# Kernel optimization log

Measured on AMD Instinct MI355X. Metric: run time of the kernel, lower is better.

The kernel has to match this reference:

```python
import jax, jax.numpy as jnp
import numpy as np

N_NODES = 50000
N_EDGES = 800000
IN_CH, HID, OUT_CH = 128, 256, 40


def setup_inputs() -> dict:
    key = jax.random.key(0)
    ks = jax.random.split(key, 10)
    x = jax.random.normal(ks[0], (N_NODES, IN_CH), dtype=jnp.float32)
    edge_index = jax.random.randint(ks[1], (2, N_EDGES), 0, N_NODES, dtype=jnp.int64)
    s = 0.05  # weight init scale
    return {
        "x": x,
        "edge_index": edge_index,
        "W1a": jax.random.normal(ks[2], (IN_CH, HID), dtype=jnp.float32) * s,
        "b1a": jnp.zeros((HID,), jnp.float32),
        "W2a": jax.random.normal(ks[3], (HID, HID), dtype=jnp.float32) * s,
        "b2a": jnp.zeros((HID,), jnp.float32),
        "W1b": jax.random.normal(ks[4], (HID, HID), dtype=jnp.float32) * s,
        "b1b": jnp.zeros((HID,), jnp.float32),
        "W2b": jax.random.normal(ks[5], (HID, HID), dtype=jnp.float32) * s,
        "b2b": jnp.zeros((HID,), jnp.float32),
        "Wlin": jax.random.normal(ks[6], (HID * 2, OUT_CH), dtype=jnp.float32) * s,
        "blin": jnp.zeros((OUT_CH,), jnp.float32),
    }


def _gin_conv(h, src, dst, W1, b1, W2, b2):
    # sum-aggregate messages h[src] into destination nodes, eps = 0
    agg = jax.ops.segment_sum(h[src], dst, num_segments=N_NODES)
    z = h + agg
    z = jnp.maximum(z @ W1 + b1, 0.0) @ W2 + b2  # 2-layer MLP
    return z


def reference(x, edge_index, W1a, b1a, W2a, b2a, W1b, b1b, W2b, b2b, Wlin, blin):
    src, dst = edge_index[0], edge_index[1]
    h1 = jnp.maximum(_gin_conv(x, src, dst, W1a, b1a, W2a, b2a), 0.0)
    h2 = jnp.maximum(_gin_conv(h1, src, dst, W1b, b1b, W2b, b2b), 0.0)
    h_cat = jnp.concatenate([h1, h2], axis=1)  # [N, 2*HID]
    logits = h_cat @ Wlin + blin
    return jax.nn.log_softmax(logits, axis=1)
```

## Files before the change

kernel.cpp:

```cpp
#include <hip/hip_runtime.h>
#include <math.h>

#define N_NODES 50000
#define N_EDGES 800000
#define IN_CH 128
#define HID 256
#define OUT_CH 40
#define GRP 6250
#define NCHUNK 64
#define TS 264

typedef unsigned short u16;
typedef unsigned char u8;
typedef __attribute__((ext_vector_type(8))) short bf16x8;
typedef __attribute__((ext_vector_type(8))) unsigned short u16x8;
typedef __attribute__((ext_vector_type(4))) float f32x4;
typedef __attribute__((ext_vector_type(2))) float f32x2;

__device__ __forceinline__ float bf2f(u16 u) {
    union { unsigned int i; float f; } v; v.i = ((unsigned int)u) << 16; return v.f;
}
__device__ __forceinline__ u16 f2bf(float f) {
    union { float f; unsigned int i; } v; v.f = f;
    unsigned int x = v.i;
    x += 0x7fffu + ((x >> 16) & 1u);
    return (u16)(x >> 16);
}

#define GLOBAL_AS __attribute__((address_space(1)))
#define LDS_AS __attribute__((address_space(3)))
__device__ __forceinline__ void async_cp16(const void* g, void* l) {
    __builtin_amdgcn_global_load_lds((const GLOBAL_AS unsigned int*)g,
                                     (LDS_AS unsigned int*)l, 16, 0, 0);
}

__device__ __forceinline__ void pack_w(
    const float* __restrict__ in, u16* __restrict__ out, int K, int N, int c)
{
    for (int k = threadIdx.x; k < K; k += 256) {
        int kk32 = k >> 5, quad = (k >> 3) & 3, e = k & 7;
        size_t base = (((size_t)c * (K >> 5) + kk32) * 64 + quad * 16) * 8 + e;
#pragma unroll
        for (int li = 0; li < 16; li++) {
            int n = c * 16 + li;
            float v = (n < N) ? in[(size_t)k * N + n] : 0.f;
            out[base + (size_t)li * 8] = f2bf(v);
        }
    }
}

__global__ __launch_bounds__(256) void prep_fused(
    const float* __restrict__ x, u16* __restrict__ xb, u8* __restrict__ xf8,
    const int* __restrict__ ei, u16* __restrict__ e16,
    const float* __restrict__ W1a, const float* __restrict__ W2a,
    const float* __restrict__ W1b, const float* __restrict__ W2b,
    const float* __restrict__ Wlin,
    u16* __restrict__ W1aPk, u16* __restrict__ W2aPk,
    u16* __restrict__ W1bPk, u16* __restrict__ W2bPk, u16* __restrict__ WlinPk)
{
    int b = blockIdx.x;
    if (b < 6250) {
        int i = b * 256 + threadIdx.x;
        float4 v = ((const float4*)x)[i];
        ushort4 o;
        o.x = f2bf(v.x); o.y = f2bf(v.y); o.z = f2bf(v.z); o.w = f2bf(v.w);
        ((ushort4*)xb)[i] = o;
        int p = __builtin_amdgcn_cvt_pk_fp8_f32(v.x, v.y, 0, false);
        p = __builtin_amdgcn_cvt_pk_fp8_f32(v.z, v.w, p, true);
        ((unsigned int*)xf8)[i] = (unsigned int)p;
    } else if (b < 7813) {
        int i = (b - 6250) * 256 + threadIdx.x;
        if (i < (2 * N_EDGES) / 4) {
            int4 v = ((const int4*)ei)[i];
            ushort4 o;
            o.x = (u16)v.x; o.y = (u16)v.y; o.z = (u16)v.z; o.w = (u16)v.w;
            ((ushort4*)e16)[i] = o;
        }
    } else {
        int t = b - 7813;
        if (t < 16)       pack_w(W1a, W1aPk, IN_CH, HID, t);
        else if (t < 32)  pack_w(W2a, W2aPk, HID, HID, t - 16);
        else if (t < 48)  pack_w(W1b, W1bPk, HID, HID, t - 32);
        else if (t < 64)  pack_w(W2b, W2bPk, HID, HID, t - 48);
        else              pack_w(Wlin, WlinPk, 2 * HID, OUT_CH, t - 64);
    }
}

__global__ __launch_bounds__(256) void hist_priv(
    const u16* __restrict__ dst16, u16* __restrict__ partial)
{
    __shared__ int hist[GRP];
    const int b = blockIdx.x;
    const int g = b & 7;
    const int sub = b >> 3;
    const int lo = g * GRP;
    const int CH = N_EDGES / NCHUNK;
    for (int i = threadIdx.x; i < GRP; i += 256) hist[i] = 0;
    __syncthreads();
    const ushort4* dsts = (const ushort4*)(dst16 + sub * CH);
    for (int k = threadIdx.x; k < CH / 4; k += 256) {
        ushort4 d = dsts[k];
        int r0 = (int)d.x - lo, r1 = (int)d.y - lo;
        int r2 = (int)d.z - lo, r3 = (int)d.w - lo;
        if ((unsigned)r0 < (unsigned)GRP) atomicAdd(&hist[r0], 1);
        if ((unsigned)r1 < (unsigned)GRP) atomicAdd(&hist[r1], 1);
        if ((unsigned)r2 < (unsigned)GRP) atomicAdd(&hist[r2], 1);
        if ((unsigned)r3 < (unsigned)GRP) atomicAdd(&hist[r3], 1);
    }
    __syncthreads();
    u16* po = partial + (size_t)b * GRP;
    for (int i = threadIdx.x; i < GRP; i += 256) po[i] = (u16)hist[i];
}

__global__ __launch_bounds__(256) void scan1(
    const u16* __restrict__ partial, int* __restrict__ excl,
    int* __restrict__ partials_out)
{
    __shared__ int lds[256];
    const int tid = threadIdx.x;
    const int base = blockIdx.x * 1024 + tid * 4;
    int v[4]; int s = 0;
#pragma unroll
    for (int i = 0; i < 4; i++) {
        int idx = base + i;
        int d = 0;
        if (idx < N_NODES) {
            int g = idx / GRP;
            int off = idx - g * GRP;
#pragma unroll
            for (int sub = 0; sub < NCHUNK; sub++)
                d += partial[(size_t)(sub * 8 + g) * GRP + off];
        }
        v[i] = d;
        s += d;
    }
    lds[tid] = s;
    __syncthreads();
    for (int off = 1; off < 256; off <<= 1) {
        int t = (tid >= off) ? lds[tid - off] : 0;
        __syncthreads();
        lds[tid] += t;
        __syncthreads();
    }
    int run = lds[tid] - s;
#pragma unroll
    for (int i = 0; i < 4; i++) {
        int idx = base + i;
        if (idx < N_NODES) excl[idx] = run;
        run += v[i];
    }
    if (tid == 255) partials_out[blockIdx.x] = lds[255];
}

__global__ __launch_bounds__(256) void scan3(
    int* __restrict__ excl, const int* __restrict__ partials,
    int* __restrict__ cursor, int nPart)
{
    __shared__ int bp[64];
    const int tid = threadIdx.x;
    if (tid < 64) {
        int orig = (tid < nPart) ? partials[tid] : 0;
        int v = orig;
#pragma unroll
        for (int off = 1; off < 64; off <<= 1) {
            int t = __shfl_up(v, off, 64);
            if (tid >= off) v += t;
        }
        bp[tid] = v - orig;
    }
    __syncthreads();
    int idx = blockIdx.x * 256 + tid;
    if (idx < N_NODES) {
        int r = excl[idx] + bp[idx >> 10];
        excl[idx] = r;
        cursor[idx] = r;
    }
}

__global__ __launch_bounds__(256) void csr_fill(
    const u16* __restrict__ src16, const u16* __restrict__ dst16,
    int* __restrict__ cursor, u16* __restrict__ csr_src)
{
    const int g = blockIdx.x & 7;
    const int c = blockIdx.x >> 3;
    const int lo = g * GRP, hi = lo + GRP;
    const int base = c * 2048;
#pragma unroll
    for (int i = 0; i < 8; i++) {
        int e = base + i * 256 + threadIdx.x;
        if (e < N_EDGES) {
            int d = dst16[e];
            if (d >= lo && d < hi) {
                int pos = atomicAdd(&cursor[d], 1);
                csr_src[pos] = src16[e];
            }
        }
    }
}


__global__ __launch_bounds__(256) void gather_agg_f8_128(
    const u16* __restrict__ feat_bf, const u8* __restrict__ feat_f8,
    const int* __restrict__ row_ptr, const int* __restrict__ row_end,
    const u16* __restrict__ csr_src, u16* __restrict__ out)
{
    const int tid = threadIdx.x;
    const int lane = tid & 63;
    const int wv = tid >> 6;
    const int li = lane & 7;
    int node = blockIdx.x * 32 + wv * 8 + (lane >> 3);
    const bool valid = node < N_NODES;
    if (!valid) node = N_NODES - 1;

    int j = row_ptr[node];
    int deg = valid ? (row_end[node] - j) : 0;

    float acc[16];
    {
        u16x8 s0 = *(const u16x8*)(feat_bf + (size_t)node * IN_CH + li * 16);
        u16x8 s1 = *(const u16x8*)(feat_bf + (size_t)node * IN_CH + li * 16 + 8);
#pragma unroll
        for (int q = 0; q < 8; q++) { acc[q] = bf2f(s0[q]); acc[8 + q] = bf2f(s1[q]); }
    }

    int maxdeg = deg;
#pragma unroll
    for (int off = 8; off < 64; off <<= 1)
        maxdeg = max(maxdeg, __shfl_xor(maxdeg, off, 64));

    for (int it = 0; it < maxdeg; it += 4) {
        int4 g0 = {0,0,0,0}, g1 = {0,0,0,0}, g2 = {0,0,0,0}, g3 = {0,0,0,0};
        if (it < deg)
            g0 = *(const int4*)(feat_f8 + (size_t)csr_src[j + it] * IN_CH + li * 16);
        if (it + 1 < deg)
            g1 = *(const int4*)(feat_f8 + (size_t)csr_src[j + it + 1] * IN_CH + li * 16);
        if (it + 2 < deg)
            g2 = *(const int4*)(feat_f8 + (size_t)csr_src[j + it + 2] * IN_CH + li * 16);
        if (it + 3 < deg)
            g3 = *(const int4*)(feat_f8 + (size_t)csr_src[j + it + 3] * IN_CH + li * 16);
#pragma unroll
        for (int q = 0; q < 4; q++) {
            int w0 = (&g0.x)[q], w1 = (&g1.x)[q], w2 = (&g2.x)[q], w3 = (&g3.x)[q];
            f32x2 l0 = __builtin_amdgcn_cvt_pk_f32_fp8(w0, false);
            f32x2 h0 = __builtin_amdgcn_cvt_pk_f32_fp8(w0, true);
            f32x2 l1 = __builtin_amdgcn_cvt_pk_f32_fp8(w1, false);
            f32x2 h1 = __builtin_amdgcn_cvt_pk_f32_fp8(w1, true);
            f32x2 l2 = __builtin_amdgcn_cvt_pk_f32_fp8(w2, false);
            f32x2 h2 = __builtin_amdgcn_cvt_pk_f32_fp8(w2, true);
            f32x2 l3 = __builtin_amdgcn_cvt_pk_f32_fp8(w3, false);
            f32x2 h3 = __builtin_amdgcn_cvt_pk_f32_fp8(w3, true);
            acc[q * 4 + 0] += (l0.x + l1.x) + (l2.x + l3.x);
            acc[q * 4 + 1] += (l0.y + l1.y) + (l2.y + l3.y);
            acc[q * 4 + 2] += (h0.x + h1.x) + (h2.x + h3.x);
            acc[q * 4 + 3] += (h0.y + h1.y) + (h2.y + h3.y);
        }
    }

    if (valid) {
        u16x8 o0, o1;
#pragma unroll
        for (int q = 0; q < 8; q++) { o0[q] = f2bf(acc[q]); o1[q] = f2bf(acc[8 + q]); }
        *(u16x8*)(out + (size_t)node * IN_CH + li * 16) = o0;
        *(u16x8*)(out + (size_t)node * IN_CH + li * 16 + 8) = o1;
    }
}

__global__ __launch_bounds__(256) void gather_agg_f8_256(
    const u16* __restrict__ feat_bf, const u8* __restrict__ feat_f8,
    const int* __restrict__ row_ptr, const int* __restrict__ row_end,
    const u16* __restrict__ csr_src, u16* __restrict__ out)
{
    const int tid = threadIdx.x;
    const int lane = tid & 63;
    const int wv = tid >> 6;
    const int li = lane & 15;
    const int node = blockIdx.x * 16 + wv * 4 + (lane >> 4);

    int j = row_ptr[node];
    int deg = row_end[node] - j;

    float acc[16];
    {
        u16x8 s0 = *(const u16x8*)(feat_bf + (size_t)node * HID + li * 16);
        u16x8 s1 = *(const u16x8*)(feat_bf + (size_t)node * HID + li * 16 + 8);
#pragma unroll
        for (int q = 0; q < 8; q++) { acc[q] = bf2f(s0[q]); acc[8 + q] = bf2f(s1[q]); }
    }

    int maxdeg = deg;
#pragma unroll
    for (int off = 16; off < 64; off <<= 1)
        maxdeg = max(maxdeg, __shfl_xor(maxdeg, off, 64));

    for (int it = 0; it < maxdeg; it += 4) {
        int4 g0 = {0,0,0,0}, g1 = {0,0,0,0}, g2 = {0,0,0,0}, g3 = {0,0,0,0};
        if (it < deg)
            g0 = *(const int4*)(feat_f8 + (size_t)csr_src[j + it] * HID + li * 16);
        if (it + 1 < deg)
            g1 = *(const int4*)(feat_f8 + (size_t)csr_src[j + it + 1] * HID + li * 16);
        if (it + 2 < deg)
            g2 = *(const int4*)(feat_f8 + (size_t)csr_src[j + it + 2] * HID + li * 16);
        if (it + 3 < deg)
            g3 = *(const int4*)(feat_f8 + (size_t)csr_src[j + it + 3] * HID + li * 16);
#pragma unroll
        for (int q = 0; q < 4; q++) {
            int w0 = (&g0.x)[q], w1 = (&g1.x)[q], w2 = (&g2.x)[q], w3 = (&g3.x)[q];
            f32x2 l0 = __builtin_amdgcn_cvt_pk_f32_fp8(w0, false);
            f32x2 h0 = __builtin_amdgcn_cvt_pk_f32_fp8(w0, true);
            f32x2 l1 = __builtin_amdgcn_cvt_pk_f32_fp8(w1, false);
            f32x2 h1 = __builtin_amdgcn_cvt_pk_f32_fp8(w1, true);
            f32x2 l2 = __builtin_amdgcn_cvt_pk_f32_fp8(w2, false);
            f32x2 h2 = __builtin_amdgcn_cvt_pk_f32_fp8(w2, true);
            f32x2 l3 = __builtin_amdgcn_cvt_pk_f32_fp8(w3, false);
            f32x2 h3 = __builtin_amdgcn_cvt_pk_f32_fp8(w3, true);
            acc[q * 4 + 0] += (l0.x + l1.x) + (l2.x + l3.x);
            acc[q * 4 + 1] += (l0.y + l1.y) + (l2.y + l3.y);
            acc[q * 4 + 2] += (h0.x + h1.x) + (h2.x + h3.x);
            acc[q * 4 + 3] += (h0.y + h1.y) + (h2.y + h3.y);
        }
    }

    u16x8 o0, o1;
#pragma unroll
    for (int q = 0; q < 8; q++) { o0[q] = f2bf(acc[q]); o1[q] = f2bf(acc[8 + q]); }
    *(u16x8*)(out + (size_t)node * HID + li * 16) = o0;
    *(u16x8*)(out + (size_t)node * HID + li * 16 + 8) = o1;
}

__global__ __launch_bounds__(256, 4) void mlp_fused(
    const u16* __restrict__ A, int K1,
    const u16* __restrict__ W1pk, const float* __restrict__ b1,
    const u16* __restrict__ W2pk, const float* __restrict__ b2,
    u16* __restrict__ out, u8* __restrict__ outF8, int M)
{
    __shared__ u16 SB[64 * TS];

    const int tid = threadIdx.x;
    const int lane = tid & 63;
    const int wid = tid >> 6;
    const int li = lane & 15;
    const int quad = lane >> 4;
    const int koff = quad * 8;
    const int row0 = blockIdx.x * 64;
    const int KB1 = K1 >> 5;
    const int rsh = (K1 == 256) ? 9 : 8;

    {
        const u8* Ag = (const u8*)(A + (size_t)row0 * K1);
        const int rounds = K1 >> 5;
        for (int j = 0; j < rounds; j++) {
            int L = (j * 256 + tid) * 16;
            int G = L ^ (((L >> rsh) & 7) << 4);
            async_cp16(Ag + G, (u8*)SB + L);
        }
    }

    f32x4 acc[4][4];
#pragma unroll
    for (int i = 0; i < 4; i++)
#pragma unroll
        for (int j = 0; j < 4; j++) acc[i][j] = (f32x4){0.f, 0.f, 0.f, 0.f};

#define LDW(WF, WPK, KB, KK32)                                                \
    {   _Pragma("unroll")                                                     \
        for (int t = 0; t < 4; t++)                                           \
            WF[t] = *(const bf16x8*)((WPK) +                                  \
                (((size_t)(wid * 4 + t) * (KB) + (KK32)) * 64 + lane) * 8); }
#define LDA1(AF, KK)                                                          \
    {   _Pragma("unroll")                                                     \
        for (int t = 0; t < 4; t++) {                                         \
            int row = t * 16 + li;                                            \
            int bo = row * (K1 * 2) + ((KK) + koff) * 2;                      \
            bo ^= (row & 7) << 4;                                             \
            AF[t] = *(const bf16x8*)((const u8*)SB + bo); } }
#define LDA2(AF, KK)                                                          \
    {   _Pragma("unroll")                                                     \
        for (int t = 0; t < 4; t++)                                           \
            AF[t] = *(const bf16x8*)(SB + (t * 16 + li) * TS + (KK) + koff); }
#define MFMA16(AF, WF)                                                        \
    {   _Pragma("unroll")                                                     \
        for (int mt = 0; mt < 4; mt++)                                        \
            _Pragma("unroll")                                                 \
            for (int nt = 0; nt < 4; nt++)                                    \
                acc[mt][nt] = __builtin_amdgcn_mfma_f32_16x16x32_bf16(        \
                    AF[mt], WF[nt], acc[mt][nt], 0, 0, 0); }

    bf16x8 wfA[4], wfB[4], af[4];

    LDW(wfA, W1pk, KB1, 0);
    __syncthreads();

    for (int kk32 = 0; kk32 < KB1; kk32 += 2) {
        LDW(wfB, W1pk, KB1, kk32 + 1);
        LDA1(af, kk32 * 32);
        MFMA16(af, wfA);
        if (kk32 + 2 < KB1) LDW(wfA, W1pk, KB1, kk32 + 2);
        LDA1(af, kk32 * 32 + 32);
        MFMA16(af, wfB);
    }
    __syncthreads();

#pragma unroll
    for (int nt = 0; nt < 4; nt++) {
        int col = wid * 64 + nt * 16 + li;
        float bv = b1[col];
#pragma unroll
        for (int mt = 0; mt < 4; mt++) {
#pragma unroll
            for (int reg = 0; reg < 4; reg++) {
                int row = mt * 16 + quad * 4 + reg;
                float v = fmaxf(acc[mt][nt][reg] + bv, 0.f);
                SB[row * TS + col] = f2bf(v);
                acc[mt][nt][reg] = 0.f;
            }
        }
    }
    LDW(wfA, W2pk, 8, 0);
    __syncthreads();

    for (int kk32 = 0; kk32 < 8; kk32 += 2) {
        LDW(wfB, W2pk, 8, kk32 + 1);
        LDA2(af, kk32 * 32);
        MFMA16(af, wfA);
        if (kk32 + 2 < 8) LDW(wfA, W2pk, 8, kk32 + 2);
        LDA2(af, kk32 * 32 + 32);
        MFMA16(af, wfB);
    }
#undef LDW
#undef LDA1
#undef LDA2
#undef MFMA16

    __syncthreads();
#pragma unroll
    for (int nt = 0; nt < 4; nt++) {
        int col = wid * 64 + nt * 16 + li;
        float bv = b2[col];
#pragma unroll
        for (int mt = 0; mt < 4; mt++) {
#pragma unroll
            for (int reg = 0; reg < 4; reg++) {
                int row = mt * 16 + quad * 4 + reg;
                float v = fmaxf(acc[mt][nt][reg] + bv, 0.f);
                SB[row * TS + col] = f2bf(v);
            }
        }
    }
    __syncthreads();
#pragma unroll
    for (int it = 0; it < 8; it++) {
        int flat = it * 4096 + tid * 16;
        int r = flat >> 9;
        int cu = (flat & 511) >> 1;
        int row = row0 + r;
        if (row < M) {
            u16x8 v = *(const u16x8*)(SB + r * TS + cu);
            *(u16x8*)(out + (size_t)row * HID + cu) = v;
            if (outF8 != nullptr) {
                int p0 = __builtin_amdgcn_cvt_pk_fp8_f32(bf2f(v[0]), bf2f(v[1]), 0, false);
                p0 = __builtin_amdgcn_cvt_pk_fp8_f32(bf2f(v[2]), bf2f(v[3]), p0, true);
                int p1 = __builtin_amdgcn_cvt_pk_fp8_f32(bf2f(v[4]), bf2f(v[5]), 0, false);
                p1 = __builtin_amdgcn_cvt_pk_fp8_f32(bf2f(v[6]), bf2f(v[7]), p1, true);
                int2 pv; pv.x = p0; pv.y = p1;
                *(int2*)(outF8 + (size_t)row * HID + cu) = pv;
            }
        }
    }
}

__global__ __launch_bounds__(256, 6) void gemm_mfma(
    const u16* __restrict__ A, const u16* __restrict__ Acat, int Ksplit, int ldA,
    const u16* __restrict__ Bpk, const float* __restrict__ bias,
    float* __restrict__ out, int M, int K)
{
    const int tid = threadIdx.x;
    const int lane = tid & 63;
    const int wid = tid >> 6;
    const int li = lane & 15;
    const int quad = lane >> 4;
    const int koff = quad * 8;
    const int row0 = blockIdx.x * 64 + wid * 16;

    f32x4 acc[3];
#pragma unroll
    for (int i = 0; i < 3; i++) acc[i] = (f32x4){0.f, 0.f, 0.f, 0.f};

    int r = row0 + li;
    const int arow = (r < M) ? r : (M - 1);
    const int KB = K >> 5;

#define LD_G(AF, BF, KK)                                                      \
    {   const u16* Ab = ((KK) >= Ksplit) ? Acat : A;                          \
        const int kb = ((KK) >= Ksplit) ? ((KK) - Ksplit) : (KK);             \
        AF = *(const bf16x8*)(Ab + (size_t)arow * ldA + kb + koff);           \
        _Pragma("unroll")                                                     \
        for (int t = 0; t < 3; t++)                                           \
            BF[t] = *(const bf16x8*)(Bpk +                                    \
                (((size_t)t * KB + ((KK) >> 5)) * 64 + lane) * 8); }
#define MFMA3(AF, BF)                                                         \
    {   _Pragma("unroll")                                                     \
        for (int nt = 0; nt < 3; nt++)                                        \
            acc[nt] = __builtin_amdgcn_mfma_f32_16x16x32_bf16(                \
                AF, BF[nt], acc[nt], 0, 0, 0); }

    {
        bf16x8 a0, b0[3], a1, b1v[3];
        LD_G(a0, b0, 0);
        for (int kk = 0; kk < K; kk += 64) {
            LD_G(a1, b1v, kk + 32);
            MFMA3(a0, b0);
            if (kk + 64 < K) LD_G(a0, b0, kk + 64);
            MFMA3(a1, b1v);
        }
    }
#undef LD_G
#undef MFMA3

    float b0v = bias[li];
    float b1s = bias[16 + li];
    float b2s = (li < 8) ? bias[32 + li] : 0.f;
#pragma unroll
    for (int reg = 0; reg < 4; reg++) {
        int row = row0 + quad * 4 + reg;
        float v0 = acc[0][reg] + b0v;
        float v1 = acc[1][reg] + b1s;
        float v2 = (li < 8) ? (acc[2][reg] + b2s) : -INFINITY;
        float m = fmaxf(fmaxf(v0, v1), v2);
#pragma unroll
        for (int off = 1; off < 16; off <<= 1)
            m = fmaxf(m, __shfl_xor(m, off, 64));
        float s = expf(v0 - m) + expf(v1 - m)
                + ((li < 8) ? expf(v2 - m) : 0.f);
#pragma unroll
        for (int off = 1; off < 16; off <<= 1)
            s += __shfl_xor(s, off, 64);
        float lg = m + logf(s);
        if (row < M) {
            out[(size_t)row * OUT_CH + li] = v0 - lg;
            out[(size_t)row * OUT_CH + 16 + li] = v1 - lg;
            if (li < 8) out[(size_t)row * OUT_CH + 32 + li] = v2 - lg;
        }
    }
}

extern "C" void kernel_launch(void* const* d_in, const int* in_sizes, int n_in,
                              void* d_out, int out_size, void* d_ws, size_t ws_size,
                              hipStream_t stream)
{
    const float* x    = (const float*)d_in[0];
    const int*   ei   = (const int*)d_in[1];
    const float* W1a  = (const float*)d_in[2];
    const float* b1a  = (const float*)d_in[3];
    const float* W2a  = (const float*)d_in[4];
    const float* b2a  = (const float*)d_in[5];
    const float* W1b  = (const float*)d_in[6];
    const float* b1b  = (const float*)d_in[7];
    const float* W2b  = (const float*)d_in[8];
    const float* b2b  = (const float*)d_in[9];
    const float* Wlin = (const float*)d_in[10];
    const float* blin = (const float*)d_in[11];
    float* out = (float*)d_out;

    const size_t R = (size_t)N_NODES * HID;
    u16* R0 = (u16*)d_ws;
    u16* R1 = R0 + R;
    u16* R2 = R1 + R;
    u16* R3 = R2 + R;
    u16* R4 = R3 + R;
    u16* xbf = R0;
    u16* zA  = R1;
    u16* partial = (u16*)R1;
    u8*  xf8 = (u8*)(R1 + (size_t)N_NODES * IN_CH);
    u8*  h1f8 = (u8*)R1;
    u16* h1  = R3;
    u16* zB  = R4;
    u16* h2  = R2;

    u16* wts = R4 + R;
    u16* W1aPk = wts;
    u16* W2aPk = W1aPk + 256 * 128;
    u16* W1bPk = W2aPk + 256 * 256;
    u16* W2bPk = W1bPk + 256 * 256;
    u16* WlinPk = W2bPk + 256 * 256;
    int* rowp   = (int*)(WlinPk + 128 * 512);
    int* cursor = rowp + N_NODES;
    int* part   = cursor + N_NODES;
    u16* csr    = (u16*)(part + 64);
    u16* e16    = csr + N_EDGES;
    u16* src16  = e16;
    u16* dst16  = e16 + N_EDGES;

    dim3 blk(256);
    const int scanBlocks = (N_NODES + 1023) / 1024;
    const int fillBlocks = 8 * ((N_EDGES + 2047) / 2048);
    const int agg128Blocks = (N_NODES + 31) / 32;
    const int agg256Blocks = N_NODES / 16;
    const int mlpBlocks  = (N_NODES + 63) / 64;
    const int gemmBlocks = (N_NODES + 63) / 64;

    prep_fused<<<7880, blk, 0, stream>>>(x, xbf, xf8, ei, e16,
                                         W1a, W2a, W1b, W2b, Wlin,
                                         W1aPk, W2aPk, W1bPk, W2bPk, WlinPk);
    hist_priv<<<8 * NCHUNK, blk, 0, stream>>>(dst16, partial);
    scan1<<<scanBlocks, blk, 0, stream>>>(partial, rowp, part);
    scan3<<<(N_NODES + 255) / 256, blk, 0, stream>>>(rowp, part, cursor, scanBlocks);
    csr_fill<<<fillBlocks, blk, 0, stream>>>(src16, dst16, cursor, csr);

    gather_agg_f8_128<<<agg128Blocks, blk, 0, stream>>>(xbf, xf8, rowp, cursor, csr, zA);
    mlp_fused<<<mlpBlocks, blk, 0, stream>>>(zA, IN_CH, W1aPk, b1a, W2aPk, b2a,
                                             h1, h1f8, N_NODES);

    gather_agg_f8_256<<<agg256Blocks, blk, 0, stream>>>(h1, h1f8, rowp, cursor, csr, zB);
    mlp_fused<<<mlpBlocks, blk, 0, stream>>>(zB, HID, W1bPk, b1b, W2bPk, b2b,
                                             h2, nullptr, N_NODES);

    gemm_mfma<<<gemmBlocks, blk, 0, stream>>>(h1, h2, HID, HID, WlinPk, blin,
                                              out, N_NODES, 2 * HID);
}
```

Baseline: 286.5 us.

## Use per-chunk prefix offsets so CSR fill atomics run in LDS

The scan kernel now records a per-chunk running prefix count for each node, so csr_fill can start each (group, chunk) block with exact local cursors held in shared memory. The global atomicAdd on a cursor array is replaced by LDS atomics, and each block reads only its chunk of edges with vectorised loads instead of scanning all edges per group. Row ends now come from rowp+1 with a sentinel written after the last node, which removes the separate cursor array. The cost is a new 64×N u16 chunk-prefix buffer written in scan1, which adds global write traffic.

```diff
diff --git a/kernel.cpp b/kernel.cpp
--- a/kernel.cpp
+++ b/kernel.cpp
@@ -114,7 +114,7 @@
 
 __global__ __launch_bounds__(256) void scan1(
     const u16* __restrict__ partial, int* __restrict__ excl,
-    int* __restrict__ partials_out)
+    int* __restrict__ partials_out, u16* __restrict__ chunkpref)
 {
     __shared__ int lds[256];
     const int tid = threadIdx.x;
@@ -128,8 +128,10 @@
             int g = idx / GRP;
             int off = idx - g * GRP;
 #pragma unroll
-            for (int sub = 0; sub < NCHUNK; sub++)
+            for (int sub = 0; sub < NCHUNK; sub++) {
+                chunkpref[(size_t)sub * N_NODES + idx] = (u16)d;
                 d += partial[(size_t)(sub * 8 + g) * GRP + off];
+            }
         }
         v[i] = d;
         s += d;
@@ -154,7 +156,7 @@
 
 __global__ __launch_bounds__(256) void scan3(
     int* __restrict__ excl, const int* __restrict__ partials,
-    int* __restrict__ cursor, int nPart)
+    int* __restrict__ sentinel, int nPart)
 {
     __shared__ int bp[64];
     const int tid = threadIdx.x;
@@ -173,28 +175,35 @@
     if (idx < N_NODES) {
         int r = excl[idx] + bp[idx >> 10];
         excl[idx] = r;
-        cursor[idx] = r;
-    }
+    }
+    if (idx == 0) sentinel[0] = N_EDGES;
 }
 
 __global__ __launch_bounds__(256) void csr_fill(
     const u16* __restrict__ src16, const u16* __restrict__ dst16,
-    int* __restrict__ cursor, u16* __restrict__ csr_src)
-{
+    const int* __restrict__ rowp, const u16* __restrict__ chunkpref,
+    u16* __restrict__ csr_src)
+{
+    __shared__ int cur[GRP];
     const int g = blockIdx.x & 7;
     const int c = blockIdx.x >> 3;
-    const int lo = g * GRP, hi = lo + GRP;
-    const int base = c * 2048;
-#pragma unroll
-    for (int i = 0; i < 8; i++) {
-        int e = base + i * 256 + threadIdx.x;
-        if (e < N_EDGES) {
-            int d = dst16[e];
-            if (d >= lo && d < hi) {
-                int pos = atomicAdd(&cursor[d], 1);
-                csr_src[pos] = src16[e];
-            }
-        }
+    const int lo = g * GRP;
+    const int CH = N_EDGES / NCHUNK;
+    const u16* cp = chunkpref + (size_t)c * N_NODES + lo;
+    for (int i = threadIdx.x; i < GRP; i += 256)
+        cur[i] = rowp[lo + i] + cp[i];
+    __syncthreads();
+    const ushort4* dsts = (const ushort4*)(dst16 + c * CH);
+    const ushort4* srcs = (const ushort4*)(src16 + c * CH);
+    for (int k = threadIdx.x; k < CH / 4; k += 256) {
+        ushort4 d = dsts[k];
+        ushort4 sc = srcs[k];
+        int r0 = (int)d.x - lo, r1 = (int)d.y - lo;
+        int r2 = (int)d.z - lo, r3 = (int)d.w - lo;
+        if ((unsigned)r0 < (unsigned)GRP) { int p = atomicAdd(&cur[r0], 1); csr_src[p] = sc.x; }
+        if ((unsigned)r1 < (unsigned)GRP) { int p = atomicAdd(&cur[r1], 1); csr_src[p] = sc.y; }
+        if ((unsigned)r2 < (unsigned)GRP) { int p = atomicAdd(&cur[r2], 1); csr_src[p] = sc.z; }
+        if ((unsigned)r3 < (unsigned)GRP) { int p = atomicAdd(&cur[r3], 1); csr_src[p] = sc.w; }
     }
 }
 
@@ -589,10 +598,10 @@
     u16* e16    = csr + N_EDGES;
     u16* src16  = e16;
     u16* dst16  = e16 + N_EDGES;
+    u16* chunkpref = dst16 + N_EDGES;
 
     dim3 blk(256);
     const int scanBlocks = (N_NODES + 1023) / 1024;
-    const int fillBlocks = 8 * ((N_EDGES + 2047) / 2048);
     const int agg128Blocks = (N_NODES + 31) / 32;
     const int agg256Blocks = N_NODES / 16;
     const int mlpBlocks  = (N_NODES + 63) / 64;
@@ -602,15 +611,15 @@
                                          W1a, W2a, W1b, W2b, Wlin,
                                          W1aPk, W2aPk, W1bPk, W2bPk, WlinPk);
     hist_priv<<<8 * NCHUNK, blk, 0, stream>>>(dst16, partial);
-    scan1<<<scanBlocks, blk, 0, stream>>>(partial, rowp, part);
+    scan1<<<scanBlocks, blk, 0, stream>>>(partial, rowp, part, chunkpref);
     scan3<<<(N_NODES + 255) / 256, blk, 0, stream>>>(rowp, part, cursor, scanBlocks);
-    csr_fill<<<fillBlocks, blk, 0, stream>>>(src16, dst16, cursor, csr);
-
-    gather_agg_f8_128<<<agg128Blocks, blk, 0, stream>>>(xbf, xf8, rowp, cursor, csr, zA);
+    csr_fill<<<8 * NCHUNK, blk, 0, stream>>>(src16, dst16, rowp, chunkpref, csr);
+
+    gather_agg_f8_128<<<agg128Blocks, blk, 0, stream>>>(xbf, xf8, rowp, rowp + 1, csr, zA);
     mlp_fused<<<mlpBlocks, blk, 0, stream>>>(zA, IN_CH, W1aPk, b1a, W2aPk, b2a,
                                              h1, h1f8, N_NODES);
 
-    gather_agg_f8_256<<<agg256Blocks, blk, 0, stream>>>(h1, h1f8, rowp, cursor, csr, zB);
+    gather_agg_f8_256<<<agg256Blocks, blk, 0, stream>>>(h1, h1f8, rowp, rowp + 1, csr, zB);
     mlp_fused<<<mlpBlocks, blk, 0, stream>>>(zB, HID, W1bPk, b1b, W2bPk, b2b,
                                              h2, nullptr, N_NODES);
 
```

Result: faster. 259.5 us (-9.4%).
